# Kernel optimization log

Measured on AMD Instinct MI355X. Metric: run time of the kernel, lower is better.

## Reference

```python
import jax, jax.numpy as jnp
import numpy as np

B, T, F, H, HORIZON = 16384, 50, 2, 64, 50


def setup_inputs() -> dict:
    key = jax.random.key(0)
    ks = jax.random.split(key, 7)
    s = 1.0 / np.sqrt(H)  # PyTorch LSTM init scale
    return {
        "history": jax.random.normal(ks[0], (B, T, F), jnp.float32),
        "W_ih": jax.random.uniform(ks[1], (4 * H, F), jnp.float32, -s, s),
        "W_hh": jax.random.uniform(ks[2], (4 * H, H), jnp.float32, -s, s),
        "b_ih": jax.random.uniform(ks[3], (4 * H,), jnp.float32, -s, s),
        "b_hh": jax.random.uniform(ks[4], (4 * H,), jnp.float32, -s, s),
        "W_dec": jax.random.uniform(ks[5], (F, H), jnp.float32, -s, s),
        "b_dec": jax.random.uniform(ks[6], (F,), jnp.float32, -s, s),
    }


def _lstm_cell(h, c, x, W_ih, W_hh, b):
    # gates in PyTorch order: input, forget, cell(g), output
    gates = x @ W_ih.T + h @ W_hh.T + b  # [B, 4H]
    i, f, g, o = jnp.split(gates, 4, axis=-1)
    c_new = jax.nn.sigmoid(f) * c + jax.nn.sigmoid(i) * jnp.tanh(g)
    h_new = jax.nn.sigmoid(o) * jnp.tanh(c_new)
    return h_new, c_new


def reference(history, W_ih, W_hh, b_ih, b_hh, W_dec, b_dec):
    b = b_ih + b_hh
    nb, hdim = history.shape[0], W_hh.shape[1]
    h0 = jnp.zeros((nb, hdim), history.dtype)
    c0 = jnp.zeros((nb, hdim), history.dtype)

    # Encode history: scan over time (xs leading axis = T)
    def enc_step(carry, x_t):
        h, c = carry
        h, c = _lstm_cell(h, c, x_t, W_ih, W_hh, b)
        return (h, c), None

    (h, c), _ = jax.lax.scan(enc_step, (h0, c0), jnp.swapaxes(history, 0, 1))

    x0 = history[:, -1, :]  # [B, F]

    def dec_step(carry, _):
        h, c, x = carry
        h, c = _lstm_cell(h, c, x, W_ih, W_hh, b)
        dxy = h @ W_dec.T + b_dec  # [B, F]
        return (h, c, dxy), dxy

    _, preds = jax.lax.scan(dec_step, (h, c, x0), None, length=HORIZON)
    return jnp.swapaxes(preds, 0, 1)  # [B, HORIZON, F]
```

## Files before the change

### kernel.cpp

```cpp
#include <hip/hip_runtime.h>

typedef __attribute__((ext_vector_type(8))) _Float16 half8;
typedef __attribute__((ext_vector_type(4))) float f32x4;
typedef __attribute__((ext_vector_type(2))) float f32x2;

#define TSTEPS 50
#define HOR    50
#define RSC    2048.0f
#define RSCI   (1.0f/2048.0f)

__device__ __forceinline__ float frcp(float x) { return __builtin_amdgcn_rcpf(x); }
__device__ __forceinline__ float sigmoidf(float x) { return frcp(1.f + __expf(-x)); }
__device__ __forceinline__ float tanh_fast(float x) {
  float ax = fabsf(x);
  float e  = __expf(-2.f * ax);
  float r  = (1.f - e) * frcp(1.f + e);
  return copysignf(r, x);
}
union HU { _Float16 h; unsigned short u; };
__device__ __forceinline__ unsigned short f2h_u(float x) { HU t; t.h = (_Float16)x; return t.u; }
__device__ __forceinline__ float h2f_u(unsigned short u) { HU t; t.u = u; return (float)t.h; }

__global__ __launch_bounds__(256, 2)
void traj_lstm_h16(const float* __restrict__ hist,
                   const float* __restrict__ W_ih,
                   const float* __restrict__ W_hh,
                   const float* __restrict__ b_ih,
                   const float* __restrict__ b_hh,
                   const float* __restrict__ W_dec,
                   const float* __restrict__ b_dec,
                   float* __restrict__ out)
{
  __shared__ unsigned short hsh0[2][32][72];
  __shared__ unsigned short hsh1[2][32][72];
  __shared__ float wdl[2][64];
  __shared__ float bdl2[2];

  const int tid  = threadIdx.x;
  const int q    = tid >> 6;
  const int lane = tid & 63;
  const int col  = lane & 15;
  const int g    = lane >> 4;
  const int batch0 = blockIdx.x * 32;

  if (tid < 128) wdl[tid >> 6][tid & 63] = W_dec[tid];
  if (tid < 2)   bdl2[tid] = b_dec[tid];
  for (int idx = tid; idx < 2 * 32 * 72; idx += 256) {
    ((unsigned short*)hsh0)[idx] = 0;
    ((unsigned short*)hsh1)[idx] = 0;
  }

  half8 wb0[4][2], wb1[4][2];
  #pragma unroll
  for (int gt = 0; gt < 4; ++gt) {
    const int row = gt * 64 + q * 16 + col;
    #pragma unroll
    for (int kq = 0; kq < 2; ++kq) {
      #pragma unroll
      for (int e = 0; e < 8; ++e) {
        float f = W_hh[row * 64 + kq * 32 + g * 8 + e];
        _Float16 h0 = (_Float16)f;
        wb0[gt][kq][e] = h0;
        wb1[gt][kq][e] = (_Float16)((f - (float)h0) * RSC);
      }
    }
  }

  float bias[4], wx[4], wy[4];
  #pragma unroll
  for (int gt = 0; gt < 4; ++gt) {
    const int row = gt * 64 + q * 16 + col;
    bias[gt] = b_ih[row] + b_hh[row];
    wx[gt]   = W_ih[row * 2];
    wy[gt]   = W_ih[row * 2 + 1];
  }

  const float* pb[2];
  pb[0] = hist + (size_t)(batch0 + 4 * g) * 100;
  pb[1] = hist + (size_t)(batch0 + 16 + 4 * g) * 100;

  float cst[2][4] = {{0.f,0.f,0.f,0.f},{0.f,0.f,0.f,0.f}};
  float p0[2] = {0.f, 0.f}, p1[2] = {0.f, 0.f};

  __syncthreads();

  for (int s = 0; s < TSTEPS + HOR; ++s) {
    const int par = s & 1;

    half8 a0[2][2], a1[2][2];
    #pragma unroll
    for (int bg = 0; bg < 2; ++bg)
      #pragma unroll
      for (int kq = 0; kq < 2; ++kq) {
        a0[bg][kq] = *(const half8*)&hsh0[par][bg * 16 + col][kq * 32 + g * 8];
        a1[bg][kq] = *(const half8*)&hsh1[par][bg * 16 + col][kq * 32 + g * 8];
      }

    float x0[2][4], x1[2][4];
    if (s <= TSTEPS) {
      #pragma unroll
      for (int bg = 0; bg < 2; ++bg)
        #pragma unroll
        for (int r = 0; r < 4; ++r) {
          f32x2 xv = *(const f32x2*)(pb[bg] + r * 100);
          x0[bg][r] = xv.x; x1[bg][r] = xv.y;
        }
      if (s < TSTEPS - 1) { pb[0] += 2; pb[1] += 2; }
    } else {
      #pragma unroll
      for (int bg = 0; bg < 2; ++bg)
        #pragma unroll
        for (int r = 0; r < 4; ++r) {
          x0[bg][r] = __shfl(p0[bg], 4 * g + r);
          x1[bg][r] = __shfl(p1[bg], 4 * g + r);
        }
    }

    f32x4 gatev[4][2];
    #pragma unroll
    for (int gt = 0; gt < 4; ++gt)
      #pragma unroll
      for (int bg = 0; bg < 2; ++bg) {
        f32x4 aH = {0.f,0.f,0.f,0.f};
        f32x4 aL = {0.f,0.f,0.f,0.f};
        aH = __builtin_amdgcn_mfma_f32_16x16x32_f16(a0[bg][0], wb0[gt][0], aH, 0, 0, 0);
        aH = __builtin_amdgcn_mfma_f32_16x16x32_f16(a0[bg][1], wb0[gt][1], aH, 0, 0, 0);
        aL = __builtin_amdgcn_mfma_f32_16x16x32_f16(a1[bg][0], wb0[gt][0], aL, 0, 0, 0);
        aL = __builtin_amdgcn_mfma_f32_16x16x32_f16(a1[bg][1], wb0[gt][1], aL, 0, 0, 0);
        aL = __builtin_amdgcn_mfma_f32_16x16x32_f16(a0[bg][0], wb1[gt][0], aL, 0, 0, 0);
        aL = __builtin_amdgcn_mfma_f32_16x16x32_f16(a0[bg][1], wb1[gt][1], aL, 0, 0, 0);
        #pragma unroll
        for (int r = 0; r < 4; ++r) gatev[gt][bg][r] = fmaf(aL[r], RSCI, aH[r]);
      }

    #pragma unroll
    for (int bg = 0; bg < 2; ++bg)
      #pragma unroll
      for (int r = 0; r < 4; ++r) {
        float gi = gatev[0][bg][r] + bias[0] + x0[bg][r] * wx[0] + x1[bg][r] * wy[0];
        float gf = gatev[1][bg][r] + bias[1] + x0[bg][r] * wx[1] + x1[bg][r] * wy[1];
        float gg = gatev[2][bg][r] + bias[2] + x0[bg][r] * wx[2] + x1[bg][r] * wy[2];
        float go = gatev[3][bg][r] + bias[3] + x0[bg][r] * wx[3] + x1[bg][r] * wy[3];
        float si = sigmoidf(gi);
        float sf = sigmoidf(gf);
        float tg = tanh_fast(gg);
        float so = sigmoidf(go);
        float cn = fmaf(sf, cst[bg][r], si * tg);
        cst[bg][r] = cn;
        float hv = so * tanh_fast(cn);
        _Float16 h0 = (_Float16)hv;
        HU t0; t0.h = h0;
        unsigned short h1u = f2h_u((hv - (float)h0) * RSC);
        const int row = bg * 16 + 4 * g + r;
        hsh0[par ^ 1][row][q * 16 + col] = t0.u;
        hsh1[par ^ 1][row][q * 16 + col] = h1u;
      }
    __syncthreads();

    if (s >= TSTEPS) {
      #pragma unroll
      for (int bg = 0; bg < 2; ++bg) {
        const unsigned short* H0 = &hsh0[par ^ 1][bg * 16 + col][g * 16];
        const unsigned short* H1 = &hsh1[par ^ 1][bg * 16 + col][g * 16];
        half8 v0a = *(const half8*)&H0[0], v0b = *(const half8*)&H0[8];
        half8 v1a = *(const half8*)&H1[0], v1b = *(const half8*)&H1[8];
        float s0 = 0.f, s1 = 0.f;
        #pragma unroll
        for (int e = 0; e < 8; ++e) {
          float hva = fmaf(RSCI, (float)v1a[e], (float)v0a[e]);
          float hvb = fmaf(RSCI, (float)v1b[e], (float)v0b[e]);
          s0 = fmaf(hva, wdl[0][g * 16 + e], s0);
          s0 = fmaf(hvb, wdl[0][g * 16 + 8 + e], s0);
          s1 = fmaf(hva, wdl[1][g * 16 + e], s1);
          s1 = fmaf(hvb, wdl[1][g * 16 + 8 + e], s1);
        }
        s0 += __shfl_xor(s0, 16); s0 += __shfl_xor(s0, 32);
        s1 += __shfl_xor(s1, 16); s1 += __shfl_xor(s1, 32);
        p0[bg] = s0 + bdl2[0];
        p1[bg] = s1 + bdl2[1];
      }
      if (q == 0 && g == 0) {
        f32x2 oa = { p0[0], p1[0] };
        f32x2 ob = { p0[1], p1[1] };
        *(f32x2*)&out[(size_t)(batch0 + col) * 100 + (size_t)(s - TSTEPS) * 2] = oa;
        *(f32x2*)&out[(size_t)(batch0 + 16 + col) * 100 + (size_t)(s - TSTEPS) * 2] = ob;
      }
    }
  }
}

extern "C" void kernel_launch(void* const* d_in, const int* in_sizes, int n_in,
                              void* d_out, int out_size, void* d_ws, size_t ws_size,
                              hipStream_t stream) {
  (void)in_sizes; (void)n_in; (void)ws_size; (void)d_ws; (void)out_size;
  const float* hist  = (const float*)d_in[0];
  const float* W_ih  = (const float*)d_in[1];
  const float* W_hh  = (const float*)d_in[2];
  const float* b_ih  = (const float*)d_in[3];
  const float* b_hh  = (const float*)d_in[4];
  const float* W_dec = (const float*)d_in[5];
  const float* b_dec = (const float*)d_in[6];
  float* out = (float*)d_out;

  dim3 grid(16384 / 32);
  dim3 block(256);
  traj_lstm_h16<<<grid, block, 0, stream>>>(hist, W_ih, W_hh, b_ih, b_hh,
                                            W_dec, b_dec, out);
}
```

Measured before the change: 370.2 us.

## Halve batch per block, move gate constants to LDS, simplify tanh

Each block now handles 16 batch rows instead of 32, which doubles the grid and raises launch bounds to 4 blocks per SIMD, trading per-step work per wave for more concurrent waves to hide the serial recurrence latency. Bias and input weights move from registers into an LDS float4 table read every step, freeing registers to allow that occupancy. Tanh is rewritten as 2/(1+e^-2x)-1, removing abs and copysign, at some risk of overflow or precision loss for large negative inputs. The history loads are now indexed directly rather than through advancing pointers.

```diff
diff --git a/kernel.cpp b/kernel.cpp
--- a/kernel.cpp
+++ b/kernel.cpp
@@ -12,17 +12,14 @@
 __device__ __forceinline__ float frcp(float x) { return __builtin_amdgcn_rcpf(x); }
 __device__ __forceinline__ float sigmoidf(float x) { return frcp(1.f + __expf(-x)); }
 __device__ __forceinline__ float tanh_fast(float x) {
-  float ax = fabsf(x);
-  float e  = __expf(-2.f * ax);
-  float r  = (1.f - e) * frcp(1.f + e);
-  return copysignf(r, x);
+  float e = __expf(-2.f * x);
+  return fmaf(2.f, frcp(1.f + e), -1.f);
 }
 union HU { _Float16 h; unsigned short u; };
 __device__ __forceinline__ unsigned short f2h_u(float x) { HU t; t.h = (_Float16)x; return t.u; }
-__device__ __forceinline__ float h2f_u(unsigned short u) { HU t; t.u = u; return (float)t.h; }
 
-__global__ __launch_bounds__(256, 2)
-void traj_lstm_h16(const float* __restrict__ hist,
+__global__ __launch_bounds__(256, 4)
+void traj_lstm_r11(const float* __restrict__ hist,
                    const float* __restrict__ W_ih,
                    const float* __restrict__ W_hh,
                    const float* __restrict__ b_ih,
@@ -31,21 +28,31 @@
                    const float* __restrict__ b_dec,
                    float* __restrict__ out)
 {
-  __shared__ unsigned short hsh0[2][32][72];
-  __shared__ unsigned short hsh1[2][32][72];
+  __shared__ unsigned short hsh0[2][16][72];
+  __shared__ unsigned short hsh1[2][16][72];
+  __shared__ f32x4 cwl[256];
   __shared__ float wdl[2][64];
-  __shared__ float bdl2[2];
+  __shared__ float bdl[2];
 
   const int tid  = threadIdx.x;
   const int q    = tid >> 6;
   const int lane = tid & 63;
   const int col  = lane & 15;
   const int g    = lane >> 4;
-  const int batch0 = blockIdx.x * 32;
+  const int batch0 = blockIdx.x * 16;
 
+  {
+    const int row = tid;
+    f32x4 cv;
+    cv.x = b_ih[row] + b_hh[row];
+    cv.y = W_ih[2 * row];
+    cv.z = W_ih[2 * row + 1];
+    cv.w = 0.f;
+    cwl[row] = cv;
+  }
   if (tid < 128) wdl[tid >> 6][tid & 63] = W_dec[tid];
-  if (tid < 2)   bdl2[tid] = b_dec[tid];
-  for (int idx = tid; idx < 2 * 32 * 72; idx += 256) {
+  if (tid < 2)   bdl[tid] = b_dec[tid];
+  for (int idx = tid; idx < 2 * 16 * 72; idx += 256) {
     ((unsigned short*)hsh0)[idx] = 0;
     ((unsigned short*)hsh1)[idx] = 0;
   }
@@ -66,124 +73,100 @@
     }
   }
 
-  float bias[4], wx[4], wy[4];
-  #pragma unroll
-  for (int gt = 0; gt < 4; ++gt) {
-    const int row = gt * 64 + q * 16 + col;
-    bias[gt] = b_ih[row] + b_hh[row];
-    wx[gt]   = W_ih[row * 2];
-    wy[gt]   = W_ih[row * 2 + 1];
-  }
-
-  const float* pb[2];
-  pb[0] = hist + (size_t)(batch0 + 4 * g) * 100;
-  pb[1] = hist + (size_t)(batch0 + 16 + 4 * g) * 100;
-
-  float cst[2][4] = {{0.f,0.f,0.f,0.f},{0.f,0.f,0.f,0.f}};
-  float p0[2] = {0.f, 0.f}, p1[2] = {0.f, 0.f};
+  float cst[4] = {0.f, 0.f, 0.f, 0.f};
+  float p0 = 0.f, p1 = 0.f;
 
   __syncthreads();
 
   for (int s = 0; s < TSTEPS + HOR; ++s) {
     const int par = s & 1;
 
-    half8 a0[2][2], a1[2][2];
+    half8 a0[2], a1[2];
     #pragma unroll
-    for (int bg = 0; bg < 2; ++bg)
+    for (int kq = 0; kq < 2; ++kq) {
+      a0[kq] = *(const half8*)&hsh0[par][col][kq * 32 + g * 8];
+      a1[kq] = *(const half8*)&hsh1[par][col][kq * 32 + g * 8];
+    }
+
+    float x0[4], x1[4];
+    if (s <= TSTEPS) {
+      const int ss = (s < TSTEPS) ? s : (TSTEPS - 1);
       #pragma unroll
-      for (int kq = 0; kq < 2; ++kq) {
-        a0[bg][kq] = *(const half8*)&hsh0[par][bg * 16 + col][kq * 32 + g * 8];
-        a1[bg][kq] = *(const half8*)&hsh1[par][bg * 16 + col][kq * 32 + g * 8];
+      for (int r = 0; r < 4; ++r) {
+        f32x2 xv = *(const f32x2*)&hist[(size_t)(batch0 + 4 * g + r) * 100 + ss * 2];
+        x0[r] = xv.x; x1[r] = xv.y;
       }
-
-    float x0[2][4], x1[2][4];
-    if (s <= TSTEPS) {
-      #pragma unroll
-      for (int bg = 0; bg < 2; ++bg)
-        #pragma unroll
-        for (int r = 0; r < 4; ++r) {
-          f32x2 xv = *(const f32x2*)(pb[bg] + r * 100);
-          x0[bg][r] = xv.x; x1[bg][r] = xv.y;
-        }
-      if (s < TSTEPS - 1) { pb[0] += 2; pb[1] += 2; }
     } else {
       #pragma unroll
-      for (int bg = 0; bg < 2; ++bg)
-        #pragma unroll
-        for (int r = 0; r < 4; ++r) {
-          x0[bg][r] = __shfl(p0[bg], 4 * g + r);
-          x1[bg][r] = __shfl(p1[bg], 4 * g + r);
-        }
+      for (int r = 0; r < 4; ++r) {
+        x0[r] = __shfl(p0, 4 * g + r);
+        x1[r] = __shfl(p1, 4 * g + r);
+      }
     }
 
-    f32x4 gatev[4][2];
+    f32x4 gatev[4];
     #pragma unroll
-    for (int gt = 0; gt < 4; ++gt)
+    for (int gt = 0; gt < 4; ++gt) {
+      f32x4 aH = {0.f,0.f,0.f,0.f};
+      f32x4 aL = {0.f,0.f,0.f,0.f};
+      aH = __builtin_amdgcn_mfma_f32_16x16x32_f16(a0[0], wb0[gt][0], aH, 0, 0, 0);
+      aH = __builtin_amdgcn_mfma_f32_16x16x32_f16(a0[1], wb0[gt][1], aH, 0, 0, 0);
+      aL = __builtin_amdgcn_mfma_f32_16x16x32_f16(a1[0], wb0[gt][0], aL, 0, 0, 0);
+      aL = __builtin_amdgcn_mfma_f32_16x16x32_f16(a1[1], wb0[gt][1], aL, 0, 0, 0);
+      aL = __builtin_amdgcn_mfma_f32_16x16x32_f16(a0[0], wb1[gt][0], aL, 0, 0, 0);
+      aL = __builtin_amdgcn_mfma_f32_16x16x32_f16(a0[1], wb1[gt][1], aL, 0, 0, 0);
       #pragma unroll
-      for (int bg = 0; bg < 2; ++bg) {
-        f32x4 aH = {0.f,0.f,0.f,0.f};
-        f32x4 aL = {0.f,0.f,0.f,0.f};
-        aH = __builtin_amdgcn_mfma_f32_16x16x32_f16(a0[bg][0], wb0[gt][0], aH, 0, 0, 0);
-        aH = __builtin_amdgcn_mfma_f32_16x16x32_f16(a0[bg][1], wb0[gt][1], aH, 0, 0, 0);
-        aL = __builtin_amdgcn_mfma_f32_16x16x32_f16(a1[bg][0], wb0[gt][0], aL, 0, 0, 0);
-        aL = __builtin_amdgcn_mfma_f32_16x16x32_f16(a1[bg][1], wb0[gt][1], aL, 0, 0, 0);
-        aL = __builtin_amdgcn_mfma_f32_16x16x32_f16(a0[bg][0], wb1[gt][0], aL, 0, 0, 0);
-        aL = __builtin_amdgcn_mfma_f32_16x16x32_f16(a0[bg][1], wb1[gt][1], aL, 0, 0, 0);
-        #pragma unroll
-        for (int r = 0; r < 4; ++r) gatev[gt][bg][r] = fmaf(aL[r], RSCI, aH[r]);
-      }
+      for (int r = 0; r < 4; ++r) gatev[gt][r] = fmaf(aL[r], RSCI, aH[r]);
+    }
+
+    f32x4 cv[4];
+    #pragma unroll
+    for (int gt = 0; gt < 4; ++gt) cv[gt] = cwl[gt * 64 + q * 16 + col];
 
     #pragma unroll
-    for (int bg = 0; bg < 2; ++bg)
-      #pragma unroll
-      for (int r = 0; r < 4; ++r) {
-        float gi = gatev[0][bg][r] + bias[0] + x0[bg][r] * wx[0] + x1[bg][r] * wy[0];
-        float gf = gatev[1][bg][r] + bias[1] + x0[bg][r] * wx[1] + x1[bg][r] * wy[1];
-        float gg = gatev[2][bg][r] + bias[2] + x0[bg][r] * wx[2] + x1[bg][r] * wy[2];
-        float go = gatev[3][bg][r] + bias[3] + x0[bg][r] * wx[3] + x1[bg][r] * wy[3];
-        float si = sigmoidf(gi);
-        float sf = sigmoidf(gf);
-        float tg = tanh_fast(gg);
-        float so = sigmoidf(go);
-        float cn = fmaf(sf, cst[bg][r], si * tg);
-        cst[bg][r] = cn;
-        float hv = so * tanh_fast(cn);
-        _Float16 h0 = (_Float16)hv;
-        HU t0; t0.h = h0;
-        unsigned short h1u = f2h_u((hv - (float)h0) * RSC);
-        const int row = bg * 16 + 4 * g + r;
-        hsh0[par ^ 1][row][q * 16 + col] = t0.u;
-        hsh1[par ^ 1][row][q * 16 + col] = h1u;
-      }
+    for (int r = 0; r < 4; ++r) {
+      float gi = gatev[0][r] + cv[0].x + x0[r] * cv[0].y + x1[r] * cv[0].z;
+      float gf = gatev[1][r] + cv[1].x + x0[r] * cv[1].y + x1[r] * cv[1].z;
+      float gg = gatev[2][r] + cv[2].x + x0[r] * cv[2].y + x1[r] * cv[2].z;
+      float go = gatev[3][r] + cv[3].x + x0[r] * cv[3].y + x1[r] * cv[3].z;
+      float si = sigmoidf(gi);
+      float sf = sigmoidf(gf);
+      float tg = tanh_fast(gg);
+      float so = sigmoidf(go);
+      float cn = fmaf(sf, cst[r], si * tg);
+      cst[r] = cn;
+      float hv = so * tanh_fast(cn);
+      _Float16 h0 = (_Float16)hv;
+      HU t0; t0.h = h0;
+      unsigned short h1u = f2h_u((hv - (float)h0) * RSC);
+      hsh0[par ^ 1][4 * g + r][q * 16 + col] = t0.u;
+      hsh1[par ^ 1][4 * g + r][q * 16 + col] = h1u;
+    }
     __syncthreads();
 
     if (s >= TSTEPS) {
+      const unsigned short* H0 = &hsh0[par ^ 1][col][g * 16];
+      const unsigned short* H1 = &hsh1[par ^ 1][col][g * 16];
+      half8 v0a = *(const half8*)&H0[0], v0b = *(const half8*)&H0[8];
+      half8 v1a = *(const half8*)&H1[0], v1b = *(const half8*)&H1[8];
+      float s0 = 0.f, s1 = 0.f;
       #pragma unroll
-      for (int bg = 0; bg < 2; ++bg) {
-        const unsigned short* H0 = &hsh0[par ^ 1][bg * 16 + col][g * 16];
-        const unsigned short* H1 = &hsh1[par ^ 1][bg * 16 + col][g * 16];
-        half8 v0a = *(const half8*)&H0[0], v0b = *(const half8*)&H0[8];
-        half8 v1a = *(const half8*)&H1[0], v1b = *(const half8*)&H1[8];
-        float s0 = 0.f, s1 = 0.f;
-        #pragma unroll
-        for (int e = 0; e < 8; ++e) {
-          float hva = fmaf(RSCI, (float)v1a[e], (float)v0a[e]);
-          float hvb = fmaf(RSCI, (float)v1b[e], (float)v0b[e]);
-          s0 = fmaf(hva, wdl[0][g * 16 + e], s0);
-          s0 = fmaf(hvb, wdl[0][g * 16 + 8 + e], s0);
-          s1 = fmaf(hva, wdl[1][g * 16 + e], s1);
-          s1 = fmaf(hvb, wdl[1][g * 16 + 8 + e], s1);
-        }
-        s0 += __shfl_xor(s0, 16); s0 += __shfl_xor(s0, 32);
-        s1 += __shfl_xor(s1, 16); s1 += __shfl_xor(s1, 32);
-        p0[bg] = s0 + bdl2[0];
-        p1[bg] = s1 + bdl2[1];
+      for (int e = 0; e < 8; ++e) {
+        float hva = fmaf(RSCI, (float)v1a[e], (float)v0a[e]);
+        float hvb = fmaf(RSCI, (float)v1b[e], (float)v0b[e]);
+        s0 = fmaf(hva, wdl[0][g * 16 + e], s0);
+        s0 = fmaf(hvb, wdl[0][g * 16 + 8 + e], s0);
+        s1 = fmaf(hva, wdl[1][g * 16 + e], s1);
+        s1 = fmaf(hvb, wdl[1][g * 16 + 8 + e], s1);
       }
+      s0 += __shfl_xor(s0, 16); s0 += __shfl_xor(s0, 32);
+      s1 += __shfl_xor(s1, 16); s1 += __shfl_xor(s1, 32);
+      p0 = s0 + bdl[0];
+      p1 = s1 + bdl[1];
+
       if (q == 0 && g == 0) {
-        f32x2 oa = { p0[0], p1[0] };
-        f32x2 ob = { p0[1], p1[1] };
-        *(f32x2*)&out[(size_t)(batch0 + col) * 100 + (size_t)(s - TSTEPS) * 2] = oa;
-        *(f32x2*)&out[(size_t)(batch0 + 16 + col) * 100 + (size_t)(s - TSTEPS) * 2] = ob;
+        f32x2 o2 = { p0, p1 };
+        *(f32x2*)&out[(size_t)(batch0 + col) * 100 + (size_t)(s - TSTEPS) * 2] = o2;
       }
     }
   }
@@ -202,8 +185,8 @@
   const float* b_dec = (const float*)d_in[6];
   float* out = (float*)d_out;
 
-  dim3 grid(16384 / 32);
+  dim3 grid(16384 / 16);
   dim3 block(256);
-  traj_lstm_h16<<<grid, block, 0, stream>>>(hist, W_ih, W_hh, b_ih, b_hh,
+  traj_lstm_r11<<<grid, block, 0, stream>>>(hist, W_ih, W_hh, b_ih, b_hh,
                                             W_dec, b_dec, out);
 }
```

After: 338.3 us. 8.6% less time.
